# Kernel tuning notes

Measured on AMD Instinct MI355X. Metric: run time of the kernel, lower is better.

## Reference

```python
import jax, jax.numpy as jnp
import numpy as np

IN, OUT, K = 512, 512, 8
BATCH = 8192
X_MIN, X_MAX, GAMMA_SCALE = 0.0, 1.0, 3.0


def setup_inputs() -> dict:
    key = jax.random.key(0)
    kx, kc = jax.random.split(key)
    x = jax.random.uniform(kx, (BATCH, IN), dtype=jnp.float32)
    coeffs = 0.01 * jax.random.normal(kc, (OUT, IN, K), dtype=jnp.float32)
    raw_alpha = jnp.zeros((IN,), jnp.float32)
    beta = jnp.zeros((IN,), jnp.float32)
    centers = jnp.broadcast_to(jnp.linspace(X_MIN, X_MAX, K, dtype=jnp.float32), (IN, K))
    delta = (X_MAX - X_MIN) / (K - 1)
    slopes = jnp.full((IN, K), GAMMA_SCALE / delta, dtype=jnp.float32)
    return {"x": x, "coeffs": coeffs, "raw_alpha": raw_alpha, "beta": beta,
            "centers": centers, "slopes": slopes}


def reference(x, coeffs, raw_alpha, beta, centers, slopes):
    # affine transform inside the basis
    alpha = jax.nn.softplus(raw_alpha) + 1e-6          # (in,)
    u = alpha[None, :] * x + beta[None, :]             # (batch, in)
    # tanh basis expansion: (batch, in, K)
    basis = 0.5 * (1.0 + jnp.tanh(slopes[None] * (u[:, :, None] - centers[None])))
    # contraction over in and basis dims == GEMM (batch, in*K) @ (in*K, out)
    y = jnp.einsum('bik,oik->bo', basis, coeffs)       # (batch, out)
    return y
```

## Files before the change

### kernel.cpp

```cpp
#include <hip/hip_runtime.h>
#include <hip/hip_bf16.h>
#include <cstdint>
#include <cstddef>

#define IN_F   512
#define OUT_F  512
#define KBASIS 8
#define BATCH  8192
#define KDIM   (IN_F * KBASIS)

#define BM 64
#define BN 256
#define BKS 64
#define NSTEPS (KDIM / BKS)
#define NTHREADS 512

typedef __attribute__((ext_vector_type(8))) short  short8;
typedef __attribute__((ext_vector_type(4))) float  f32x4;

static __device__ __forceinline__ unsigned short f2bf16(float f) {
    union { float f; unsigned u; } v; v.f = f;
    unsigned u = v.u;
    return (unsigned short)((u + 0x7FFFu + ((u >> 16) & 1u)) >> 16);
}

__global__ void prep_kakb(const float* __restrict__ raw_alpha,
                          const float* __restrict__ beta,
                          const float* __restrict__ centers,
                          const float* __restrict__ slopes,
                          float* __restrict__ ka, float* __restrict__ kb) {
    int idx = blockIdx.x * blockDim.x + threadIdx.x;
    if (idx >= KDIM) return;
    int i = idx >> 3;
    float ra = raw_alpha[i];
    float sp = (ra > 20.f) ? ra : log1pf(expf(ra));
    float alpha = sp + 1e-6f;
    float s = slopes[idx];
    float c = centers[idx];
    const float NEG2LOG2E = -2.8853900817779268f;
    ka[idx] = NEG2LOG2E * s * alpha;
    kb[idx] = NEG2LOG2E * s * (beta[i] - c);
}

__global__ void prep_wb(const float* __restrict__ w,
                        unsigned short* __restrict__ wb, int n4) {
    int idx = blockIdx.x * blockDim.x + threadIdx.x;
    if (idx >= n4) return;
    float4 v = *(const float4*)(w + (size_t)idx * 4);
    ushort4 r;
    r.x = f2bf16(v.x); r.y = f2bf16(v.y); r.z = f2bf16(v.z); r.w = f2bf16(v.w);
    *(ushort4*)(wb + (size_t)idx * 4) = r;
}

__global__ __launch_bounds__(NTHREADS, 2)
void fused_tanh_gemm(const float* __restrict__ x,
                     const unsigned short* __restrict__ Wb,
                     const float* __restrict__ ka,
                     const float* __restrict__ kb,
                     float* __restrict__ out) {
    __shared__ unsigned short As[2][BM][BKS];
    __shared__ unsigned short Bs[2][BN][BKS];

    const int tid  = threadIdx.x;
    const int wid  = tid >> 6;
    const int lane = tid & 63;

    const int bid = blockIdx.x;
    const int bm0 = (bid >> 1) * BM;
    const int bn0 = (bid & 1) * BN;

    const int am = tid >> 3;
    const int ac = tid & 7;
    const float* xrow = x + (size_t)(bm0 + am) * IN_F;

    const int wr = wid >> 2;
    const int wc = wid & 3;
    const int fr = lane & 15;
    const int fq = lane >> 4;

    auto stageB = [&](int b, int t) {
        const int kd0 = t * BKS;
        #pragma unroll
        for (int j = 0; j < 4; ++j) {
            int q  = wid * 256 + j * 64 + lane;
            int op = q >> 3;
            int cs = (q & 7) ^ (op & 7);
            const unsigned short* src = Wb + (size_t)(bn0 + op) * KDIM + kd0 + cs * 8;
            unsigned short* ldsbase = &Bs[b][0][0] + (wid * 4 + j) * 512;
            __builtin_amdgcn_global_load_lds(
                (const __attribute__((address_space(1))) void*)src,
                (__attribute__((address_space(3))) void*)ldsbase,
                16, 0, 0);
        }
    };

    auto stageA = [&](int b, int t) {
        const int ai = t * 8 + ac;
        float xv = xrow[ai];
        f32x4 a0 = *(const f32x4*)(ka + ai * 8);
        f32x4 a1 = *(const f32x4*)(ka + ai * 8 + 4);
        f32x4 b0 = *(const f32x4*)(kb + ai * 8);
        f32x4 b1 = *(const f32x4*)(kb + ai * 8 + 4);
        short8 pk;
        #pragma unroll
        for (int k = 0; k < 4; ++k) {
            float p0 = a0[k] * xv + b0[k];
            float p1 = a1[k] * xv + b1[k];
            float e0 = __builtin_amdgcn_exp2f(p0);
            float e1 = __builtin_amdgcn_exp2f(p1);
            pk[k]     = (short)f2bf16(__builtin_amdgcn_rcpf(1.0f + e0));
            pk[k + 4] = (short)f2bf16(__builtin_amdgcn_rcpf(1.0f + e1));
        }
        ((short8*)&As[b][am][0])[ac ^ (am & 7)] = pk;
    };

    auto computeTile = [&](int b, f32x4 acc[2][4]) {
        #pragma unroll
        for (int kh = 0; kh < 2; ++kh) {
            short8 afrag[2], bfrag[4];
            #pragma unroll
            for (int mi = 0; mi < 2; ++mi) {
                int row = wr * 32 + mi * 16 + fr;
                afrag[mi] = ((const short8*)&As[b][row][0])[(kh * 4 + fq) ^ (row & 7)];
            }
            #pragma unroll
            for (int ni = 0; ni < 4; ++ni) {
                int orow = wc * 64 + ni * 16 + fr;
                bfrag[ni] = ((const short8*)&Bs[b][orow][0])[(kh * 4 + fq) ^ (orow & 7)];
            }
            #pragma unroll
            for (int mi = 0; mi < 2; ++mi)
                #pragma unroll
                for (int ni = 0; ni < 4; ++ni)
                    acc[mi][ni] = __builtin_amdgcn_mfma_f32_16x16x32_bf16(
                        afrag[mi], bfrag[ni], acc[mi][ni], 0, 0, 0);
        }
    };

    f32x4 acc[2][4];
    #pragma unroll
    for (int mi = 0; mi < 2; ++mi)
        #pragma unroll
        for (int ni = 0; ni < 4; ++ni)
            acc[mi][ni] = (f32x4){0.f, 0.f, 0.f, 0.f};

    stageB(0, 0);
    stageA(0, 0);
    asm volatile("s_waitcnt vmcnt(0)" ::: "memory");
    __syncthreads();

    int buf = 0;
    for (int t = 0; t < NSTEPS; ++t) {
        if (t + 1 < NSTEPS) {
            stageB(buf ^ 1, t + 1);
            stageA(buf ^ 1, t + 1);
        }
        computeTile(buf, acc);
        asm volatile("s_waitcnt vmcnt(0)" ::: "memory");
        __syncthreads();
        buf ^= 1;
    }

    #pragma unroll
    for (int mi = 0; mi < 2; ++mi) {
        #pragma unroll
        for (int ni = 0; ni < 4; ++ni) {
            f32x4 v = acc[mi][ni];
            int r0  = bm0 + wr * 32 + mi * 16 + fq * 4;
            int col = bn0 + wc * 64 + ni * 16 + fr;
            #pragma unroll
            for (int j = 0; j < 4; ++j)
                out[(size_t)(r0 + j) * OUT_F + col] = v[j];
        }
    }
}

extern "C" void kernel_launch(void* const* d_in, const int* in_sizes, int n_in,
                              void* d_out, int out_size, void* d_ws, size_t ws_size,
                              hipStream_t stream) {
    const float* x         = (const float*)d_in[0];
    const float* coeffs    = (const float*)d_in[1];
    const float* raw_alpha = (const float*)d_in[2];
    const float* beta      = (const float*)d_in[3];
    const float* centers   = (const float*)d_in[4];
    const float* slopes    = (const float*)d_in[5];
    float* out = (float*)d_out;

    unsigned short* Wb = (unsigned short*)d_ws;
    float* ka = (float*)((char*)d_ws + (size_t)OUT_F * KDIM * 2);
    float* kb = ka + KDIM;

    prep_kakb<<<dim3((KDIM + 255) / 256), dim3(256), 0, stream>>>(
        raw_alpha, beta, centers, slopes, ka, kb);

    const int n4 = OUT_F * KDIM / 4;
    prep_wb<<<dim3(n4 / 256), dim3(256), 0, stream>>>(coeffs, Wb, n4);

    fused_tanh_gemm<<<dim3((BATCH / BM) * (OUT_F / BN)), dim3(NTHREADS), 0, stream>>>(
        x, Wb, ka, kb, out);
}
```

Before: 160.7 us.

## Triple-buffer B tiles, split K across warps, remap blocks per XCD

B tiles now use a three-stage ring, with global-to-LDS loads issued two steps ahead and waits relaxed to partial vmcnt counts. The x values are prefetched in registers several steps early. Warps now split the K dimension within each 64-wide tile (ks) instead of splitting M, so each warp holds a full 64x64 accumulator and the two partial sums are combined through LDS in the epilogue. Block indices are remapped so blocks on the same XCD share B columns and contiguous rows, aiming for better L2 locality. This raises the LDS footprint and register pressure and adds a reduction pass, and the out-of-range loads wrap around with masked indexing.

```diff
diff --git a/kernel.cpp b/kernel.cpp
--- a/kernel.cpp
+++ b/kernel.cpp
@@ -14,6 +14,12 @@
 #define BKS 64
 #define NSTEPS (KDIM / BKS)
 #define NTHREADS 512
+
+#define AS_STRIDE (64*64*2)
+#define BS_STRIDE (256*64*2)
+#define AS_BYTES (2*AS_STRIDE)
+#define BS_BYTES (3*BS_STRIDE)
+#define SMEM_BYTES (AS_BYTES + BS_BYTES)
 
 typedef __attribute__((ext_vector_type(8))) short  short8;
 typedef __attribute__((ext_vector_type(4))) float  f32x4;
@@ -58,35 +64,40 @@
                      const float* __restrict__ ka,
                      const float* __restrict__ kb,
                      float* __restrict__ out) {
-    __shared__ unsigned short As[2][BM][BKS];
-    __shared__ unsigned short Bs[2][BN][BKS];
+    __shared__ char smem[SMEM_BYTES];
+    unsigned short* AsBase = (unsigned short*)smem;
+    unsigned short* BsBase = (unsigned short*)(smem + AS_BYTES);
+    float* red = (float*)smem;
 
     const int tid  = threadIdx.x;
     const int wid  = tid >> 6;
     const int lane = tid & 63;
 
     const int bid = blockIdx.x;
-    const int bm0 = (bid >> 1) * BM;
-    const int bn0 = (bid & 1) * BN;
+    const int xcd = bid & 7;
+    const int rix = bid >> 3;
+    const int bn0 = (xcd & 1) * BN;
+    const int bm0 = ((xcd >> 1) * 32 + rix) * BM;
 
     const int am = tid >> 3;
     const int ac = tid & 7;
     const float* xrow = x + (size_t)(bm0 + am) * IN_F;
 
-    const int wr = wid >> 2;
     const int wc = wid & 3;
+    const int ks = wid >> 2;
     const int fr = lane & 15;
     const int fq = lane >> 4;
 
-    auto stageB = [&](int b, int t) {
+    auto stageB = [&](int buf, int t) {
         const int kd0 = t * BKS;
+        unsigned short* bb = BsBase + buf * (256 * 64);
         #pragma unroll
         for (int j = 0; j < 4; ++j) {
             int q  = wid * 256 + j * 64 + lane;
             int op = q >> 3;
             int cs = (q & 7) ^ (op & 7);
             const unsigned short* src = Wb + (size_t)(bn0 + op) * KDIM + kd0 + cs * 8;
-            unsigned short* ldsbase = &Bs[b][0][0] + (wid * 4 + j) * 512;
+            unsigned short* ldsbase = bb + (wid * 4 + j) * 512;
             __builtin_amdgcn_global_load_lds(
                 (const __attribute__((address_space(1))) void*)src,
                 (__attribute__((address_space(3))) void*)ldsbase,
@@ -94,9 +105,8 @@
         }
     };
 
-    auto stageA = [&](int b, int t) {
+    auto stageA = [&](int buf, int t, float xv) {
         const int ai = t * 8 + ac;
-        float xv = xrow[ai];
         f32x4 a0 = *(const f32x4*)(ka + ai * 8);
         f32x4 a1 = *(const f32x4*)(ka + ai * 8 + 4);
         f32x4 b0 = *(const f32x4*)(kb + ai * 8);
@@ -111,67 +121,96 @@
             pk[k]     = (short)f2bf16(__builtin_amdgcn_rcpf(1.0f + e0));
             pk[k + 4] = (short)f2bf16(__builtin_amdgcn_rcpf(1.0f + e1));
         }
-        ((short8*)&As[b][am][0])[ac ^ (am & 7)] = pk;
+        unsigned short* arow = AsBase + buf * (64 * 64) + am * 64;
+        ((short8*)arow)[ac ^ (am & 7)] = pk;
     };
 
-    auto computeTile = [&](int b, f32x4 acc[2][4]) {
-        #pragma unroll
-        for (int kh = 0; kh < 2; ++kh) {
-            short8 afrag[2], bfrag[4];
+    f32x4 acc[4][4];
+    #pragma unroll
+    for (int mi = 0; mi < 4; ++mi)
+        #pragma unroll
+        for (int ni = 0; ni < 4; ++ni)
+            acc[mi][ni] = (f32x4){0.f, 0.f, 0.f, 0.f};
+
+    auto computeTile = [&](int abuf, int bbuf) {
+        const unsigned short* ab = AsBase + abuf * (64 * 64);
+        const unsigned short* bb = BsBase + bbuf * (256 * 64);
+        short8 afrag[4], bfrag[4];
+        #pragma unroll
+        for (int mi = 0; mi < 4; ++mi) {
+            int row = mi * 16 + fr;
+            afrag[mi] = ((const short8*)(ab + row * 64))[(ks * 4 + fq) ^ (row & 7)];
+        }
+        #pragma unroll
+        for (int ni = 0; ni < 4; ++ni) {
+            int orow = wc * 64 + ni * 16 + fr;
+            bfrag[ni] = ((const short8*)(bb + orow * 64))[(ks * 4 + fq) ^ (orow & 7)];
+        }
+        #pragma unroll
+        for (int mi = 0; mi < 4; ++mi)
             #pragma unroll
-            for (int mi = 0; mi < 2; ++mi) {
-                int row = wr * 32 + mi * 16 + fr;
-                afrag[mi] = ((const short8*)&As[b][row][0])[(kh * 4 + fq) ^ (row & 7)];
-            }
+            for (int ni = 0; ni < 4; ++ni)
+                acc[mi][ni] = __builtin_amdgcn_mfma_f32_16x16x32_bf16(
+                    afrag[mi], bfrag[ni], acc[mi][ni], 0, 0, 0);
+    };
+
+    float xv0 = xrow[0 * 8 + ac];
+    float xc  = xrow[1 * 8 + ac];
+    float xn  = xrow[2 * 8 + ac];
+    stageB(0, 0);
+    stageB(1, 1);
+    stageA(0, 0, xv0);
+    asm volatile("s_waitcnt vmcnt(4) lgkmcnt(0)" ::: "memory");
+    __builtin_amdgcn_s_barrier();
+
+    int ab = 0;
+    int bb = 0;
+    for (int t = 0; t < NSTEPS; ++t) {
+        int b2 = bb + 2; if (b2 >= 3) b2 -= 3;
+        float xl = xrow[((t + 3) & (NSTEPS - 1)) * 8 + ac];
+        stageB(b2, (t + 2) & (NSTEPS - 1));
+        stageA(ab ^ 1, (t + 1) & (NSTEPS - 1), xc);
+        computeTile(ab, bb);
+        xc = xn; xn = xl;
+        asm volatile("s_waitcnt vmcnt(5) lgkmcnt(0)" ::: "memory");
+        __builtin_amdgcn_s_barrier();
+        ab ^= 1;
+        bb = (bb == 2) ? 0 : bb + 1;
+    }
+
+    asm volatile("s_waitcnt vmcnt(0) lgkmcnt(0)" ::: "memory");
+    __builtin_amdgcn_s_barrier();
+
+    if (ks == 1) {
+        #pragma unroll
+        for (int mi = 0; mi < 4; ++mi)
             #pragma unroll
             for (int ni = 0; ni < 4; ++ni) {
-                int orow = wc * 64 + ni * 16 + fr;
-                bfrag[ni] = ((const short8*)&Bs[b][orow][0])[(kh * 4 + fq) ^ (orow & 7)];
+                f32x4 v = acc[mi][ni];
+                #pragma unroll
+                for (int j = 0; j < 4; ++j) {
+                    int row = mi * 16 + fq * 4 + j;
+                    int col = ni * 16 + fr;
+                    red[(wc * 64 + row) * 64 + col] = v[j];
+                }
             }
+    }
+    asm volatile("s_waitcnt lgkmcnt(0)" ::: "memory");
+    __builtin_amdgcn_s_barrier();
+    if (ks == 0) {
+        #pragma unroll
+        for (int mi = 0; mi < 4; ++mi)
             #pragma unroll
-            for (int mi = 0; mi < 2; ++mi)
+            for (int ni = 0; ni < 4; ++ni) {
+                f32x4 v = acc[mi][ni];
                 #pragma unroll
-                for (int ni = 0; ni < 4; ++ni)
-                    acc[mi][ni] = __builtin_amdgcn_mfma_f32_16x16x32_bf16(
-                        afrag[mi], bfrag[ni], acc[mi][ni], 0, 0, 0);
-        }
-    };
-
-    f32x4 acc[2][4];
-    #pragma unroll
-    for (int mi = 0; mi < 2; ++mi)
-        #pragma unroll
-        for (int ni = 0; ni < 4; ++ni)
-            acc[mi][ni] = (f32x4){0.f, 0.f, 0.f, 0.f};
-
-    stageB(0, 0);
-    stageA(0, 0);
-    asm volatile("s_waitcnt vmcnt(0)" ::: "memory");
-    __syncthreads();
-
-    int buf = 0;
-    for (int t = 0; t < NSTEPS; ++t) {
-        if (t + 1 < NSTEPS) {
-            stageB(buf ^ 1, t + 1);
-            stageA(buf ^ 1, t + 1);
-        }
-        computeTile(buf, acc);
-        asm volatile("s_waitcnt vmcnt(0)" ::: "memory");
-        __syncthreads();
-        buf ^= 1;
-    }
-
-    #pragma unroll
-    for (int mi = 0; mi < 2; ++mi) {
-        #pragma unroll
-        for (int ni = 0; ni < 4; ++ni) {
-            f32x4 v = acc[mi][ni];
-            int r0  = bm0 + wr * 32 + mi * 16 + fq * 4;
-            int col = bn0 + wc * 64 + ni * 16 + fr;
-            #pragma unroll
-            for (int j = 0; j < 4; ++j)
-                out[(size_t)(r0 + j) * OUT_F + col] = v[j];
-        }
+                for (int j = 0; j < 4; ++j) {
+                    int row = mi * 16 + fq * 4 + j;
+                    int col = ni * 16 + fr;
+                    float s = v[j] + red[(wc * 64 + row) * 64 + col];
+                    out[(size_t)(bm0 + row) * OUT_F + bn0 + wc * 64 + col] = s;
+                }
+            }
     }
 }
 
```

After: 160.5 us. About the same (-0.1%).
